# Optimization experiments

Measured on AMD Instinct MI355X. Metric: run time of the kernel, lower is better.

The kernel has to match this reference:

```python
import jax, jax.numpy as jnp
import numpy as np

EPS = 1e-6
N_HEADS = 16
KV_HEADS = 4
HEAD_DIM = 64
N_REP = N_HEADS // KV_HEADS
N_EXPERTS = 8
TOP_K = 2


def _rms_norm(x, w):
    return x * jax.lax.rsqrt(jnp.mean(x * x, axis=-1, keepdims=True) + EPS) * w


def _apply_rope(x, fc):
    # x: (B,T,H,D); fc: (T, D//2, 2) holding (cos, sin)
    B, T, H, D = x.shape
    xr = x.reshape(B, T, H, D // 2, 2)
    f = fc.reshape(1, T, 1, D // 2, 2)
    re = xr[..., 0] * f[..., 0] - xr[..., 1] * f[..., 1]
    im = xr[..., 1] * f[..., 0] + xr[..., 0] * f[..., 1]
    return jnp.stack([re, im], axis=-1).reshape(B, T, H, D)


def _silu(x):
    return x * jax.nn.sigmoid(x)


def setup_inputs():
    key = jax.random.key(0)
    ks = jax.random.split(key, 16)
    B, T, C = 4, 1024, 1024
    IE, IS = 1024, 2048  # expert_inter_dim, shared inter_dim
    s = 0.02
    x = jax.random.normal(ks[0], (B, T, C), jnp.float32)
    inv_freq = 1.0 / (10000.0 ** (np.arange(0, HEAD_DIM, 2, dtype=np.float32) / HEAD_DIM))
    ang = np.outer(np.arange(T, dtype=np.float32), inv_freq)
    freq_cis = jnp.asarray(np.stack([np.cos(ang), np.sin(ang)], axis=-1), jnp.float32)
    causal = np.tril(np.ones((T, T), dtype=bool))
    mask = jnp.asarray(np.where(causal, 0.0, -1e9), dtype=jnp.float32).reshape(1, 1, T, T)
    window = jnp.zeros((1, 1, T, T), jnp.float32)
    return {
        "x": x,
        "freq_cis": freq_cis,
        "mask": mask,
        "window": window,
        "norm1_w": jnp.ones((C,), jnp.float32),
        "wq": jax.random.normal(ks[1], (N_HEADS * HEAD_DIM, C), jnp.float32) * s,
        "wk": jax.random.normal(ks[2], (KV_HEADS * HEAD_DIM, C), jnp.float32) * s,
        "wv": jax.random.normal(ks[3], (KV_HEADS * HEAD_DIM, C), jnp.float32) * s,
        "wo": jax.random.normal(ks[4], (C, N_HEADS * HEAD_DIM), jnp.float32) * s,
        "norm2_w": jnp.ones((C,), jnp.float32),
        "gate_w": jax.random.normal(ks[5], (N_EXPERTS, C), jnp.float32) * s,
        "exp_w1": jax.random.normal(ks[6], (N_EXPERTS, IE, C), jnp.float32) * s,
        "exp_w2": jax.random.normal(ks[7], (N_EXPERTS, IE, C), jnp.float32) * s,
        "exp_wp": jax.random.normal(ks[8], (N_EXPERTS, C, IE), jnp.float32) * s,
        "sh_w1": jax.random.normal(ks[9], (IS, C), jnp.float32) * s,
        "sh_w2": jax.random.normal(ks[10], (IS, C), jnp.float32) * s,
        "sh_wp": jax.random.normal(ks[11], (C, IS), jnp.float32) * s,
        "start_pos": 0,
    }


def reference(x, freq_cis, mask, window, norm1_w, wq, wk, wv, wo, norm2_w,
              gate_w, exp_w1, exp_w2, exp_wp, sh_w1, sh_w2, sh_wp, start_pos):
    B, T, C = x.shape
    # ---- pre-norm attention (GQA, Global mask, eval: no dropout) ----
    xn = _rms_norm(x, norm1_w)
    q = (xn @ wq.T).reshape(B, T, N_HEADS, HEAD_DIM)
    k = (xn @ wk.T).reshape(B, T, KV_HEADS, HEAD_DIM)
    v = (xn @ wv.T).reshape(B, T, KV_HEADS, HEAD_DIM)
    q = _apply_rope(q, freq_cis)
    k = _apply_rope(k, freq_cis)
    k = jnp.repeat(k, N_REP, axis=2)  # (B,T,H,D)
    v = jnp.repeat(v, N_REP, axis=2)
    scale = 1.0 / np.sqrt(HEAD_DIM).astype(np.float32)
    att = jnp.einsum("bqhd,bkhd->bhqk", q, k) * scale + mask
    p = jax.nn.softmax(att, axis=-1)
    o = jnp.einsum("bhqk,bkhd->bqhd", p, v).reshape(B, T, C)
    x = x + o @ wo.T
    # ---- pre-norm MoE FFN ----
    xn2 = _rms_norm(x, norm2_w).reshape(-1, C)  # (N,C)
    scores = xn2 @ gate_w.T                      # gate logits, returned
    probs = jax.nn.softmax(scores, axis=-1)
    top_w, top_i = jax.lax.top_k(probs, TOP_K)   # (N,K)
    # dense combine weights (N,E): zero for non-selected experts
    wfull = jnp.sum(jax.nn.one_hot(top_i, N_EXPERTS, dtype=x.dtype) * top_w[..., None], axis=1)
    h = _silu(jnp.einsum("nc,eic->eni", xn2, exp_w1)) * jnp.einsum("nc,eic->eni", xn2, exp_w2)
    ye = jnp.einsum("eni,eci->enc", h, exp_wp)   # per-expert outputs
    y = jnp.einsum("ne,enc->nc", wfull, ye)      # routed combine
    z = (_silu(xn2 @ sh_w1.T) * (xn2 @ sh_w2.T)) @ sh_wp.T  # shared expert
    out = x + (y + z).reshape(B, T, C)
    return out, scores
```

## Files before the change

### kernel.cpp

```cpp
#include <hip/hip_runtime.h>


typedef __bf16 bf16_t;
typedef __bf16 bf16x8 __attribute__((ext_vector_type(8)));
typedef __bf16 bf16x4 __attribute__((ext_vector_type(4)));
typedef float  f32x4  __attribute__((ext_vector_type(4)));

#define LQKV 1536

#define GLD16(gp, lp) __builtin_amdgcn_global_load_lds(                         \
    (const __attribute__((address_space(1))) void*)(gp),                        \
    (__attribute__((address_space(3))) void*)(lp), 16, 0, 0)

#define PIPE_BARRIER() do {                                                     \
    asm volatile("s_waitcnt vmcnt(0)" ::: "memory");                            \
    __builtin_amdgcn_s_barrier();                                               \
} while (0)

__global__ __launch_bounds__(256) void convert_k(
    const float* __restrict__ src, bf16_t* __restrict__ dst)
{
    size_t i = (size_t)blockIdx.x * 256 + threadIdx.x;
    float4 v = *((const float4*)src + i);
    bf16x4 o;
    o[0] = (bf16_t)v.x; o[1] = (bf16_t)v.y; o[2] = (bf16_t)v.z; o[3] = (bf16_t)v.w;
    *((bf16x4*)dst + i) = o;
}

struct Cvt8 {
    const float* s[8];
    bf16_t* d[8];
    int cum[9];
    int nseg;
};

__global__ __launch_bounds__(256) void convert_multi_k(Cvt8 j)
{
    int blk = blockIdx.x;
    int seg = 0;
    while (seg + 1 < j.nseg && blk >= j.cum[seg + 1]) ++seg;
    size_t i = (size_t)(blk - j.cum[seg]) * 256 + threadIdx.x;
    float4 v = *((const float4*)j.s[seg] + i);
    bf16x4 o;
    o[0] = (bf16_t)v.x; o[1] = (bf16_t)v.y; o[2] = (bf16_t)v.z; o[3] = (bf16_t)v.w;
    *((bf16x4*)j.d[seg] + i) = o;
}

__global__ __launch_bounds__(256) void gemm_bt(
    const bf16_t* __restrict__ A, const bf16_t* __restrict__ W,
    int M, int N, int K, int ldw, int mode,
    float* __restrict__ outF, bf16_t* __restrict__ outB,
    const float* __restrict__ resF, float* __restrict__ outF2)
{
    __shared__ __align__(16) bf16_t sA[2][128 * 64];
    __shared__ __align__(16) bf16_t sB[2][128 * 64];
    const int tid  = threadIdx.x;
    const int bm   = blockIdx.y * 128, bn = blockIdx.x * 128;
    const int lane = tid & 63;
    const int wv   = tid >> 6;
    const int wm   = (wv >> 1) * 64, wn = (wv & 1) * 64;
    const int lr   = lane & 15;
    const int kg   = lane >> 4;
    const int swz  = (lr & 7) << 3;

    f32x4 acc[4][4];
    #pragma unroll
    for (int i = 0; i < 4; ++i)
        #pragma unroll
        for (int j = 0; j < 4; ++j)
            acc[i][j] = f32x4{0.f, 0.f, 0.f, 0.f};

    auto STAGE = [&](int b, int k0) {
        #pragma unroll
        for (int p = 0; p < 4; ++p) {
            int idx = p * 256 + tid;
            int row = idx >> 3;
            int ch  = ((idx & 7) * 8) ^ ((row & 7) << 3);
            GLD16(A + (size_t)(bm + row) * K   + k0 + ch, sA[b] + idx * 8);
            GLD16(W + (size_t)(bn + row) * ldw + k0 + ch, sB[b] + idx * 8);
        }
    };

    STAGE(0, 0);
    PIPE_BARRIER();
    int cur = 0;
    for (int k0 = 0; k0 < K; k0 += 64) {
        if (k0 + 64 < K) STAGE(cur ^ 1, k0 + 64);
        #pragma unroll
        for (int ks = 0; ks < 2; ++ks) {
            bf16x8 af[4], bfr[4];
            #pragma unroll
            for (int i = 0; i < 4; ++i)
                af[i] = *(const bf16x8*)(sA[cur] + (wm + i * 16 + lr) * 64 +
                                         ((ks * 32 + kg * 8) ^ swz));
            #pragma unroll
            for (int j = 0; j < 4; ++j)
                bfr[j] = *(const bf16x8*)(sB[cur] + (wn + j * 16 + lr) * 64 +
                                          ((ks * 32 + kg * 8) ^ swz));
            #pragma unroll
            for (int i = 0; i < 4; ++i)
                #pragma unroll
                for (int j = 0; j < 4; ++j)
                    acc[i][j] = __builtin_amdgcn_mfma_f32_16x16x32_bf16(
                        af[i], bfr[j], acc[i][j], 0, 0, 0);
        }
        PIPE_BARRIER();
        cur ^= 1;
    }

    #pragma unroll
    for (int i = 0; i < 4; ++i) {
        #pragma unroll
        for (int j = 0; j < 4; ++j) {
            #pragma unroll
            for (int rr = 0; rr < 4; ++rr) {
                int m = bm + wm + i * 16 + kg * 4 + rr;
                int n = bn + wn + j * 16 + lr;
                size_t o = (size_t)m * N + n;
                float v = acc[i][j][rr];
                if (mode == 0)      outF[o] = v;
                else if (mode == 1) outB[o] = (bf16_t)v;
                else if (mode == 2) {
                    float r = v + resF[o];
                    outF[o] = r;
                    if (outF2) outF2[o] = r;
                } else              outF[o] += v;
            }
        }
    }
}

__global__ __launch_bounds__(256) void gemm_glu(
    const bf16_t* __restrict__ A, const bf16_t* __restrict__ W1,
    const bf16_t* __restrict__ W2, int M, int N, int K,
    bf16_t* __restrict__ out)
{
    __shared__ __align__(16) bf16_t sA[2][128 * 64];
    __shared__ __align__(16) bf16_t sB1[2][128 * 64];
    __shared__ __align__(16) bf16_t sB2[2][128 * 64];
    const int tid  = threadIdx.x;
    const int bm   = blockIdx.y * 128, bn = blockIdx.x * 128;
    const int lane = tid & 63;
    const int wv   = tid >> 6;
    const int wm   = (wv >> 1) * 64, wn = (wv & 1) * 64;
    const int lr   = lane & 15;
    const int kg   = lane >> 4;
    const int swz  = (lr & 7) << 3;

    f32x4 acc1[4][4], acc2[4][4];
    #pragma unroll
    for (int i = 0; i < 4; ++i)
        #pragma unroll
        for (int j = 0; j < 4; ++j) {
            acc1[i][j] = f32x4{0.f, 0.f, 0.f, 0.f};
            acc2[i][j] = f32x4{0.f, 0.f, 0.f, 0.f};
        }

    auto STAGE = [&](int b, int k0) {
        #pragma unroll
        for (int p = 0; p < 4; ++p) {
            int idx = p * 256 + tid;
            int row = idx >> 3;
            int ch  = ((idx & 7) * 8) ^ ((row & 7) << 3);
            GLD16(A  + (size_t)(bm + row) * K + k0 + ch, sA[b]  + idx * 8);
            GLD16(W1 + (size_t)(bn + row) * K + k0 + ch, sB1[b] + idx * 8);
            GLD16(W2 + (size_t)(bn + row) * K + k0 + ch, sB2[b] + idx * 8);
        }
    };

    STAGE(0, 0);
    PIPE_BARRIER();
    int cur = 0;
    for (int k0 = 0; k0 < K; k0 += 64) {
        if (k0 + 64 < K) STAGE(cur ^ 1, k0 + 64);
        #pragma unroll
        for (int ks = 0; ks < 2; ++ks) {
            bf16x8 af[4], b1[4], b2[4];
            #pragma unroll
            for (int i = 0; i < 4; ++i)
                af[i] = *(const bf16x8*)(sA[cur] + (wm + i * 16 + lr) * 64 +
                                         ((ks * 32 + kg * 8) ^ swz));
            #pragma unroll
            for (int j = 0; j < 4; ++j) {
                b1[j] = *(const bf16x8*)(sB1[cur] + (wn + j * 16 + lr) * 64 +
                                         ((ks * 32 + kg * 8) ^ swz));
                b2[j] = *(const bf16x8*)(sB2[cur] + (wn + j * 16 + lr) * 64 +
                                         ((ks * 32 + kg * 8) ^ swz));
            }
            #pragma unroll
            for (int i = 0; i < 4; ++i)
                #pragma unroll
                for (int j = 0; j < 4; ++j) {
                    acc1[i][j] = __builtin_amdgcn_mfma_f32_16x16x32_bf16(
                        af[i], b1[j], acc1[i][j], 0, 0, 0);
                    acc2[i][j] = __builtin_amdgcn_mfma_f32_16x16x32_bf16(
                        af[i], b2[j], acc2[i][j], 0, 0, 0);
                }
        }
        PIPE_BARRIER();
        cur ^= 1;
    }

    #pragma unroll
    for (int i = 0; i < 4; ++i) {
        #pragma unroll
        for (int j = 0; j < 4; ++j) {
            #pragma unroll
            for (int rr = 0; rr < 4; ++rr) {
                int m = bm + wm + i * 16 + kg * 4 + rr;
                int n = bn + wn + j * 16 + lr;
                float v1 = acc1[i][j][rr], v2 = acc2[i][j][rr];
                out[(size_t)m * N + n] = (bf16_t)(v1 / (1.f + __expf(-v1)) * v2);
            }
        }
    }
}

__device__ __forceinline__ int seg_off(const int* cnt, int e)
{
    int r = 0;
    #pragma unroll
    for (int k = 0; k < 8; ++k) if (k < e) r += (cnt[k] + 127) & ~127;
    return r;
}

__global__ __launch_bounds__(256) void glu_gather(
    const bf16_t* __restrict__ A, const bf16_t* __restrict__ W1,
    const bf16_t* __restrict__ W2, const int* __restrict__ tok_list,
    const int* __restrict__ cnt, bf16_t* __restrict__ h)
{
    const int e = blockIdx.y >> 5, t = blockIdx.y & 31;
    const int ce = cnt[e];
    if (t * 128 >= ce) return;
    const int hbase = seg_off(cnt, e) + t * 128;
    const bf16_t* W1e = W1 + (size_t)e * 1048576;
    const bf16_t* W2e = W2 + (size_t)e * 1048576;

    __shared__ __align__(16) bf16_t sA[2][128 * 64];
    __shared__ __align__(16) bf16_t sB1[2][128 * 64];
    __shared__ __align__(16) bf16_t sB2[2][128 * 64];
    const int tid  = threadIdx.x;
    const int bn   = blockIdx.x * 128;
    const int lane = tid & 63;
    const int wv   = tid >> 6;
    const int wm   = (wv >> 1) * 64, wn = (wv & 1) * 64;
    const int lr   = lane & 15;
    const int kg   = lane >> 4;
    const int swz  = (lr & 7) << 3;

    int tok4[4];
    #pragma unroll
    for (int p = 0; p < 4; ++p)
        tok4[p] = tok_list[e * 4096 + t * 128 + ((p * 256 + tid) >> 3)];

    f32x4 acc1[4][4], acc2[4][4];
    #pragma unroll
    for (int i = 0; i < 4; ++i)
        #pragma unroll
        for (int j = 0; j < 4; ++j) {
            acc1[i][j] = f32x4{0.f, 0.f, 0.f, 0.f};
            acc2[i][j] = f32x4{0.f, 0.f, 0.f, 0.f};
        }

    auto STAGE = [&](int b, int k0) {
        #pragma unroll
        for (int p = 0; p < 4; ++p) {
            int idx = p * 256 + tid;
            int row = idx >> 3;
            int ch  = ((idx & 7) * 8) ^ ((row & 7) << 3);
            GLD16(A   + (size_t)tok4[p] * 1024 + k0 + ch,    sA[b]  + idx * 8);
            GLD16(W1e + (size_t)(bn + row) * 1024 + k0 + ch, sB1[b] + idx * 8);
            GLD16(W2e + (size_t)(bn + row) * 1024 + k0 + ch, sB2[b] + idx * 8);
        }
    };

    STAGE(0, 0);
    PIPE_BARRIER();
    int cur = 0;
    for (int k0 = 0; k0 < 1024; k0 += 64) {
        if (k0 + 64 < 1024) STAGE(cur ^ 1, k0 + 64);
        #pragma unroll
        for (int ks = 0; ks < 2; ++ks) {
            bf16x8 af[4], b1[4], b2[4];
            #pragma unroll
            for (int i = 0; i < 4; ++i)
                af[i] = *(const bf16x8*)(sA[cur] + (wm + i * 16 + lr) * 64 +
                                         ((ks * 32 + kg * 8) ^ swz));
            #pragma unroll
            for (int j = 0; j < 4; ++j) {
                b1[j] = *(const bf16x8*)(sB1[cur] + (wn + j * 16 + lr) * 64 +
                                         ((ks * 32 + kg * 8) ^ swz));
                b2[j] = *(const bf16x8*)(sB2[cur] + (wn + j * 16 + lr) * 64 +
                                         ((ks * 32 + kg * 8) ^ swz));
            }
            #pragma unroll
            for (int i = 0; i < 4; ++i)
                #pragma unroll
                for (int j = 0; j < 4; ++j) {
                    acc1[i][j] = __builtin_amdgcn_mfma_f32_16x16x32_bf16(
                        af[i], b1[j], acc1[i][j], 0, 0, 0);
                    acc2[i][j] = __builtin_amdgcn_mfma_f32_16x16x32_bf16(
                        af[i], b2[j], acc2[i][j], 0, 0, 0);
                }
        }
        PIPE_BARRIER();
        cur ^= 1;
    }

    #pragma unroll
    for (int i = 0; i < 4; ++i) {
        #pragma unroll
        for (int j = 0; j < 4; ++j) {
            #pragma unroll
            for (int rr = 0; rr < 4; ++rr) {
                int rl = wm + i * 16 + kg * 4 + rr;
                int n  = bn + wn + j * 16 + lr;
                float v1 = acc1[i][j][rr], v2 = acc2[i][j][rr];
                h[(size_t)(hbase + rl) * 1024 + n] =
                    (bf16_t)(v1 / (1.f + __expf(-v1)) * v2);
            }
        }
    }
}

__global__ __launch_bounds__(256) void down_gather(
    const bf16_t* __restrict__ h, const bf16_t* __restrict__ Wp,
    const int* __restrict__ tok_list, const float* __restrict__ w_list,
    const int* __restrict__ cnt, float* __restrict__ out)
{
    const int e = blockIdx.y >> 5, t = blockIdx.y & 31;
    const int ce = cnt[e];
    if (t * 128 >= ce) return;
    const int hbase = seg_off(cnt, e) + t * 128;
    const bf16_t* We = Wp + (size_t)e * 1048576;

    __shared__ __align__(16) bf16_t sA[2][128 * 64];
    __shared__ __align__(16) bf16_t sB[2][128 * 64];
    const int tid  = threadIdx.x;
    const int bn   = blockIdx.x * 128;
    const int lane = tid & 63;
    const int wv   = tid >> 6;
    const int wm   = (wv >> 1) * 64, wn = (wv & 1) * 64;
    const int lr   = lane & 15;
    const int kg   = lane >> 4;
    const int swz  = (lr & 7) << 3;

    f32x4 acc[4][4];
    #pragma unroll
    for (int i = 0; i < 4; ++i)
        #pragma unroll
        for (int j = 0; j < 4; ++j)
            acc[i][j] = f32x4{0.f, 0.f, 0.f, 0.f};

    auto STAGE = [&](int b, int k0) {
        #pragma unroll
        for (int p = 0; p < 4; ++p) {
            int idx = p * 256 + tid;
            int row = idx >> 3;
            int ch  = ((idx & 7) * 8) ^ ((row & 7) << 3);
            GLD16(h  + (size_t)(hbase + row) * 1024 + k0 + ch, sA[b] + idx * 8);
            GLD16(We + (size_t)(bn + row) * 1024 + k0 + ch,    sB[b] + idx * 8);
        }
    };

    STAGE(0, 0);
    PIPE_BARRIER();
    int cur = 0;
    for (int k0 = 0; k0 < 1024; k0 += 64) {
        if (k0 + 64 < 1024) STAGE(cur ^ 1, k0 + 64);
        #pragma unroll
        for (int ks = 0; ks < 2; ++ks) {
            bf16x8 af[4], bfr[4];
            #pragma unroll
            for (int i = 0; i < 4; ++i)
                af[i] = *(const bf16x8*)(sA[cur] + (wm + i * 16 + lr) * 64 +
                                         ((ks * 32 + kg * 8) ^ swz));
            #pragma unroll
            for (int j = 0; j < 4; ++j)
                bfr[j] = *(const bf16x8*)(sB[cur] + (wn + j * 16 + lr) * 64 +
                                          ((ks * 32 + kg * 8) ^ swz));
            #pragma unroll
            for (int i = 0; i < 4; ++i)
                #pragma unroll
                for (int j = 0; j < 4; ++j)
                    acc[i][j] = __builtin_amdgcn_mfma_f32_16x16x32_bf16(
                        af[i], bfr[j], acc[i][j], 0, 0, 0);
        }
        PIPE_BARRIER();
        cur ^= 1;
    }

    #pragma unroll
    for (int i = 0; i < 4; ++i) {
        #pragma unroll
        for (int rr = 0; rr < 4; ++rr) {
            int g = t * 128 + wm + i * 16 + kg * 4 + rr;
            if (g < ce) {
                int   tok = tok_list[e * 4096 + g];
                float wgt = w_list[e * 4096 + g];
                #pragma unroll
                for (int j = 0; j < 4; ++j) {
                    int n = bn + wn + j * 16 + lr;
                    atomicAdd(&out[(size_t)tok * 1024 + n], wgt * acc[i][j][rr]);
                }
            }
        }
    }
}

__global__ __launch_bounds__(256) void rmsnorm_k(
    const float* __restrict__ src, const float* __restrict__ w,
    bf16_t* __restrict__ dst)
{
    const int row = blockIdx.x, tid = threadIdx.x;
    float4 t4 = *((const float4*)src + (size_t)row * 256 + tid);
    float ssum = t4.x*t4.x + t4.y*t4.y + t4.z*t4.z + t4.w*t4.w;
    #pragma unroll
    for (int off = 32; off > 0; off >>= 1) ssum += __shfl_down(ssum, off);
    __shared__ float red[4];
    if ((tid & 63) == 0) red[tid >> 6] = ssum;
    __syncthreads();
    float total = red[0] + red[1] + red[2] + red[3];
    float rms = rsqrtf(total * (1.0f / 1024.0f) + 1e-6f);
    float4 w4 = *((const float4*)w + tid);
    bf16x4 o4;
    o4[0] = (bf16_t)(t4.x * rms * w4.x);
    o4[1] = (bf16_t)(t4.y * rms * w4.y);
    o4[2] = (bf16_t)(t4.z * rms * w4.z);
    o4[3] = (bf16_t)(t4.w * rms * w4.w);
    *((bf16x4*)dst + (size_t)row * 256 + tid) = o4;
}

__global__ __launch_bounds__(256) void rmsnorm_gate_k(
    const float* __restrict__ src, const float* __restrict__ w,
    const float* __restrict__ gw, bf16_t* __restrict__ dst,
    float* __restrict__ scores, int* __restrict__ topi,
    float* __restrict__ topw)
{
    const int row = blockIdx.x, tid = threadIdx.x;
    float4 t4 = *((const float4*)src + (size_t)row * 256 + tid);
    float ssum = t4.x*t4.x + t4.y*t4.y + t4.z*t4.z + t4.w*t4.w;
    #pragma unroll
    for (int off = 32; off > 0; off >>= 1) ssum += __shfl_down(ssum, off);
    __shared__ float red[4];
    if ((tid & 63) == 0) red[tid >> 6] = ssum;
    __syncthreads();
    float total = red[0] + red[1] + red[2] + red[3];
    float rms = rsqrtf(total * (1.0f / 1024.0f) + 1e-6f);
    float4 w4 = *((const float4*)w + tid);
    float4 f4;
    f4.x = t4.x * rms * w4.x;
    f4.y = t4.y * rms * w4.y;
    f4.z = t4.z * rms * w4.z;
    f4.w = t4.w * rms * w4.w;
    bf16x4 o4;
    o4[0] = (bf16_t)f4.x; o4[1] = (bf16_t)f4.y;
    o4[2] = (bf16_t)f4.z; o4[3] = (bf16_t)f4.w;
    *((bf16x4*)dst + (size_t)row * 256 + tid) = o4;

    float a[8];
    #pragma unroll
    for (int e = 0; e < 8; ++e) {
        float4 g4 = *((const float4*)(gw + (size_t)e * 1024) + tid);
        a[e] = f4.x * g4.x + f4.y * g4.y + f4.z * g4.z + f4.w * g4.w;
    }
    #pragma unroll
    for (int e = 0; e < 8; ++e)
        #pragma unroll
        for (int off = 32; off > 0; off >>= 1) a[e] += __shfl_down(a[e], off);
    __shared__ float gred[4][8];
    if ((tid & 63) == 0)
        #pragma unroll
        for (int e = 0; e < 8; ++e) gred[tid >> 6][e] = a[e];
    __syncthreads();
    if (tid == 0) {
        float lg[8];
        #pragma unroll
        for (int e = 0; e < 8; ++e)
            lg[e] = gred[0][e] + gred[1][e] + gred[2][e] + gred[3][e];
        #pragma unroll
        for (int e = 0; e < 8; ++e) scores[(size_t)row * 8 + e] = lg[e];
        float mx = lg[0];
        #pragma unroll
        for (int e = 1; e < 8; ++e) mx = fmaxf(mx, lg[e]);
        float p[8], sum = 0.f;
        #pragma unroll
        for (int e = 0; e < 8; ++e) { p[e] = __expf(lg[e] - mx); sum += p[e]; }
        float inv = 1.0f / sum;
        #pragma unroll
        for (int e = 0; e < 8; ++e) p[e] *= inv;
        int i1 = 0;
        #pragma unroll
        for (int e = 1; e < 8; ++e) if (p[e] > p[i1]) i1 = e;
        int i2 = (i1 == 0) ? 1 : 0;
        #pragma unroll
        for (int e = 0; e < 8; ++e) if (e != i1 && p[e] > p[i2]) i2 = e;
        topi[row] = i1 | (i2 << 8);
        topw[row * 2]     = p[i1];
        topw[row * 2 + 1] = p[i2];
    }
}

__global__ __launch_bounds__(256) void build_lists_k(
    const int* __restrict__ topi, const float* __restrict__ topw,
    int* __restrict__ tok_list, float* __restrict__ w_list,
    int* __restrict__ cnt)
{
    const int e = blockIdx.x;
    const int tid = threadIdx.x, lane = tid & 63, wv = tid >> 6;
    __shared__ int wc[4];
    int base = 0;
    for (int t0 = 0; t0 < 4096; t0 += 256) {
        int tok = t0 + tid;
        int ti = topi[tok];
        int i1 = ti & 255, i2 = (ti >> 8) & 255;
        bool m = (i1 == e) || (i2 == e);
        unsigned long long b = __ballot(m);
        if (lane == 0) wc[wv] = __popcll(b);
        __syncthreads();
        int pos = base;
        #pragma unroll
        for (int k = 0; k < 4; ++k) if (k < wv) pos += wc[k];
        pos += __popcll(b & ((1ull << lane) - 1ull));
        if (m) {
            tok_list[e * 4096 + pos] = tok;
            w_list[e * 4096 + pos]   = (i1 == e) ? topw[tok * 2] : topw[tok * 2 + 1];
        }
        base += wc[0] + wc[1] + wc[2] + wc[3];
        __syncthreads();
    }
    int padded = (base + 127) & ~127;
    for (int p = base + tid; p < padded; p += 256) tok_list[e * 4096 + p] = 0;
    if (tid == 0) cnt[e] = base;
}

__global__ __launch_bounds__(256) void rope_all_k(
    bf16_t* __restrict__ qkv, const float* __restrict__ fc)
{
    int idx = blockIdx.x * 256 + threadIdx.x;
    int pr = idx & 31;
    int hn = idx >> 5;
    int h  = hn % 20;
    int n  = hn / 20;
    int tpos = n & 1023;
    const float* f = fc + ((size_t)tpos * 32 + pr) * 2;
    float c = f[0], s = f[1];
    int col = (h < 16) ? h * 64 : 1024 + (h - 16) * 64;
    size_t base = (size_t)n * LQKV + col + pr * 2;
    float x0 = (float)qkv[base], x1 = (float)qkv[base + 1];
    qkv[base]     = (bf16_t)(x0 * c - x1 * s);
    qkv[base + 1] = (bf16_t)(x1 * c + x0 * s);
}

__global__ __launch_bounds__(256) void transpose_v(
    const bf16_t* __restrict__ qkv, bf16_t* __restrict__ vt)
{
    __shared__ bf16_t tile[64][72];
    const int tt = blockIdx.x, kvh = blockIdx.y, b = blockIdx.z;
    const int tid = threadIdx.x;
    {
        int r = tid >> 2, c = (tid & 3) * 16;
        const bf16_t* src = qkv + ((size_t)(b * 1024 + tt * 64 + r)) * LQKV
                            + 1280 + kvh * 64 + c;
        bf16x8 v0 = *(const bf16x8*)src;
        bf16x8 v1 = *(const bf16x8*)(src + 8);
        *(bf16x8*)&tile[r][c] = v0;
        *(bf16x8*)&tile[r][c + 8] = v1;
    }
    __syncthreads();
    {
        int d = tid >> 2, t4 = (tid & 3) * 16;
        bf16_t* dst = vt + ((size_t)((b * 4 + kvh) * 64 + d)) * 1024 + tt * 64 + t4;
        bf16x8 o0, o1;
        #pragma unroll
        for (int u = 0; u < 8; ++u) {
            o0[u] = tile[t4 + u][d];
            o1[u] = tile[t4 + 8 + u][d];
        }
        *(bf16x8*)dst = o0;
        *(bf16x8*)(dst + 8) = o1;
    }
}

__global__ __launch_bounds__(256) void attn_mfma(
    const bf16_t* __restrict__ qkv, const bf16_t* __restrict__ vt,
    bf16_t* __restrict__ ob)
{
    const int qt = blockIdx.x, h = blockIdx.y, b = blockIdx.z;
    const int kvh = h >> 2;
    __shared__ __align__(16) bf16_t sK[64 * 64];
    __shared__ __align__(16) bf16_t sVt[64 * 64];
    __shared__ __align__(16) bf16_t sP[64 * 72];
    const int tid  = threadIdx.x;
    const int w    = tid >> 6;
    const int lane = tid & 63;
    const int lr   = lane & 15;
    const int kg   = lane >> 4;
    const int swz  = (lr & 7) << 3;

    bf16x8 qf[2];
    {
        const bf16_t* qrow = qkv + ((size_t)(b * 1024 + qt * 64 + w * 16 + lr)) * LQKV
                             + h * 64;
        qf[0] = *(const bf16x8*)(qrow + kg * 8);
        qf[1] = *(const bf16x8*)(qrow + 32 + kg * 8);
    }
    float m_run[4], l_run[4];
    f32x4 o_acc[4];
    #pragma unroll
    for (int rr = 0; rr < 4; ++rr) { m_run[rr] = -1.0e30f; l_run[rr] = 0.f; }
    #pragma unroll
    for (int dt = 0; dt < 4; ++dt) o_acc[dt] = f32x4{0.f, 0.f, 0.f, 0.f};

    for (int kt = 0; kt <= qt; ++kt) {
        #pragma unroll
        for (int p = 0; p < 2; ++p) {
            int idx = p * 256 + tid;
            int row = idx >> 3;
            int chs = ((idx & 7) * 8) ^ ((row & 7) << 3);
            GLD16(qkv + ((size_t)(b * 1024 + kt * 64 + row)) * LQKV
                      + 1024 + kvh * 64 + chs, sK + idx * 8);
            GLD16(vt + ((size_t)((b * 4 + kvh) * 64 + row)) * 1024 + kt * 64 + chs,
                  sVt + idx * 8);
        }
        __syncthreads();

        f32x4 sfr[4];
        #pragma unroll
        for (int j = 0; j < 4; ++j) {
            sfr[j] = f32x4{0.f, 0.f, 0.f, 0.f};
            #pragma unroll
            for (int ks = 0; ks < 2; ++ks) {
                bf16x8 bf = *(const bf16x8*)(sK + (j * 16 + lr) * 64 +
                                             ((ks * 32 + kg * 8) ^ swz));
                sfr[j] = __builtin_amdgcn_mfma_f32_16x16x32_bf16(qf[ks], bf, sfr[j], 0, 0, 0);
            }
        }
        const int rowg = qt * 64 + w * 16 + kg * 4;
        float mnew[4];
        #pragma unroll
        for (int rr = 0; rr < 4; ++rr) mnew[rr] = m_run[rr];
        #pragma unroll
        for (int j = 0; j < 4; ++j) {
            int colg = kt * 64 + j * 16 + lr;
            #pragma unroll
            for (int rr = 0; rr < 4; ++rr) {
                float s = sfr[j][rr] * 0.125f;
                if (colg > rowg + rr) s = -1.0e30f;
                sfr[j][rr] = s;
                mnew[rr] = fmaxf(mnew[rr], s);
            }
        }
        #pragma unroll
        for (int off = 1; off < 16; off <<= 1)
            #pragma unroll
            for (int rr = 0; rr < 4; ++rr)
                mnew[rr] = fmaxf(mnew[rr], __shfl_xor(mnew[rr], off, 64));
        float alpha[4], lpart[4];
        #pragma unroll
        for (int rr = 0; rr < 4; ++rr) {
            alpha[rr] = __expf(m_run[rr] - mnew[rr]);
            lpart[rr] = 0.f;
        }
        #pragma unroll
        for (int j = 0; j < 4; ++j)
            #pragma unroll
            for (int rr = 0; rr < 4; ++rr) {
                float p = __expf(sfr[j][rr] - mnew[rr]);
                sfr[j][rr] = p;
                lpart[rr] += p;
            }
        #pragma unroll
        for (int j = 0; j < 4; ++j)
            #pragma unroll
            for (int rr = 0; rr < 4; ++rr)
                sP[(w * 16 + kg * 4 + rr) * 72 + j * 16 + lr] = (bf16_t)sfr[j][rr];
        #pragma unroll
        for (int off = 1; off < 16; off <<= 1)
            #pragma unroll
            for (int rr = 0; rr < 4; ++rr)
                lpart[rr] += __shfl_xor(lpart[rr], off, 64);
        #pragma unroll
        for (int rr = 0; rr < 4; ++rr) {
            l_run[rr] = l_run[rr] * alpha[rr] + lpart[rr];
            m_run[rr] = mnew[rr];
        }
        #pragma unroll
        for (int dt = 0; dt < 4; ++dt)
            #pragma unroll
            for (int rr = 0; rr < 4; ++rr)
                o_acc[dt][rr] *= alpha[rr];
        #pragma unroll
        for (int ks = 0; ks < 2; ++ks) {
            bf16x8 af = *(const bf16x8*)(sP + (w * 16 + lr) * 72 + ks * 32 + kg * 8);
            #pragma unroll
            for (int dt = 0; dt < 4; ++dt) {
                bf16x8 bf = *(const bf16x8*)(sVt + (dt * 16 + lr) * 64 +
                                             ((ks * 32 + kg * 8) ^ swz));
                o_acc[dt] = __builtin_amdgcn_mfma_f32_16x16x32_bf16(af, bf, o_acc[dt], 0, 0, 0);
            }
        }
        __syncthreads();
    }

    float inv[4];
    #pragma unroll
    for (int rr = 0; rr < 4; ++rr) inv[rr] = 1.0f / l_run[rr];
    #pragma unroll
    for (int dt = 0; dt < 4; ++dt)
        #pragma unroll
        for (int rr = 0; rr < 4; ++rr) {
            int tok = qt * 64 + w * 16 + kg * 4 + rr;
            ob[((size_t)(b * 1024 + tok)) * 1024 + h * 64 + dt * 16 + lr] =
                (bf16_t)(o_acc[dt][rr] * inv[rr]);
        }
}

extern "C" void kernel_launch(void* const* d_in, const int* in_sizes, int n_in,
                              void* d_out, int out_size, void* d_ws, size_t ws_size,
                              hipStream_t stream)
{
    const float* x   = (const float*)d_in[0];
    const float* fc  = (const float*)d_in[1];
    const float* n1w = (const float*)d_in[4];
    const float* wq  = (const float*)d_in[5];
    const float* wk  = (const float*)d_in[6];
    const float* wv  = (const float*)d_in[7];
    const float* wo  = (const float*)d_in[8];
    const float* n2w = (const float*)d_in[9];
    const float* gw  = (const float*)d_in[10];
    const float* ew1 = (const float*)d_in[11];
    const float* ew2 = (const float*)d_in[12];
    const float* ewp = (const float*)d_in[13];
    const float* sw1 = (const float*)d_in[14];
    const float* sw2 = (const float*)d_in[15];
    const float* swp = (const float*)d_in[16];

    const size_t MB = 1024 * 1024;
    char* ws = (char*)d_ws;
    bf16_t* xnb  = (bf16_t*)(ws + 0);
    float*  x1   = (float*) (ws + 8 * MB);
    bf16_t* ew2b = (bf16_t*)(ws + 8 * MB);
    bf16_t* h    = (bf16_t*)(ws + 24 * MB);
    char*   lists= ws + 42 * MB;
    int*    tok_list = (int*)lists;
    float*  w_list   = (float*)(lists + 131072);
    int*    cnt      = (int*)(lists + 262144);
    int*    topi     = (int*)(lists + 262400);
    float*  topw     = (float*)(lists + 278784);
    bf16_t* sw1b = (bf16_t*)(ws + 43 * MB);
    bf16_t* sw2b = (bf16_t*)(ws + 47 * MB);
    bf16_t* swpb = (bf16_t*)(ws + 51 * MB);
    char*   slotA= ws + 55 * MB;
    bf16_t* hb   = (bf16_t*)slotA;
    bf16_t* qkv  = (bf16_t*)(ws + 71 * MB);
    bf16_t* ob   = (bf16_t*)(ws + 83 * MB);
    bf16_t* vt   = (bf16_t*)(ws + 91 * MB);
    bf16_t* ew1b = (bf16_t*)(ws + 71 * MB);
    bf16_t* ewpb = (bf16_t*)(ws + 71 * MB);

    float* outp   = (float*)d_out;
    float* scores = outp + (size_t)4096 * 1024;

    auto gemm = [&](const bf16_t* A, const bf16_t* W, int M, int N, int K, int ldw,
                    int mode, float* oF, bf16_t* oB, const float* res, float* oF2) {
        gemm_bt<<<dim3(N / 128, M / 128), 256, 0, stream>>>(
            A, W, M, N, K, ldw, mode, oF, oB, res, oF2);
    };

    bf16_t* wqb = (bf16_t*)slotA;
    bf16_t* wkb = wqb + 1048576;
    bf16_t* wvb = wkb + 262144;
    bf16_t* wob = wvb + 262144;
    {
        Cvt8 j;
        j.s[0]=wq;  j.d[0]=wqb;  j.s[1]=wk;  j.d[1]=wkb;
        j.s[2]=wv;  j.d[2]=wvb;  j.s[3]=wo;  j.d[3]=wob;
        j.s[4]=sw1; j.d[4]=sw1b; j.s[5]=sw2; j.d[5]=sw2b;
        j.s[6]=swp; j.d[6]=swpb; j.s[7]=nullptr; j.d[7]=nullptr;
        int sz[7] = {1024, 256, 256, 1024, 2048, 2048, 2048};
        j.cum[0] = 0;
        for (int k = 0; k < 7; ++k) j.cum[k + 1] = j.cum[k] + sz[k];
        j.cum[8] = j.cum[7];
        j.nseg = 7;
        convert_multi_k<<<j.cum[7], 256, 0, stream>>>(j);
    }

    rmsnorm_k<<<4096, 256, 0, stream>>>(x, n1w, xnb);
    gemm(xnb, wqb, 4096, LQKV, 1024, 1024, 1, nullptr, qkv, nullptr, nullptr);
    rope_all_k<<<(4096 * 20 * 32) / 256, 256, 0, stream>>>(qkv, fc);
    transpose_v<<<dim3(16, 4, 4), 256, 0, stream>>>(qkv, vt);
    attn_mfma<<<dim3(16, 16, 4), 256, 0, stream>>>(qkv, vt, ob);
    gemm(ob, wob, 4096, 1024, 1024, 1024, 2, x1, nullptr, x, outp);

    rmsnorm_gate_k<<<4096, 256, 0, stream>>>(x1, n2w, gw, xnb, scores, topi, topw);
    build_lists_k<<<8, 256, 0, stream>>>(topi, topw, tok_list, w_list, cnt);

    {
        Cvt8 j;
        j.s[0]=ew1; j.d[0]=ew1b; j.s[1]=ew2; j.d[1]=ew2b;
        for (int k = 2; k < 8; ++k) { j.s[k]=nullptr; j.d[k]=nullptr; }
        j.cum[0] = 0; j.cum[1] = 8192; j.cum[2] = 16384;
        for (int k = 3; k < 9; ++k) j.cum[k] = 16384;
        j.nseg = 2;
        convert_multi_k<<<16384, 256, 0, stream>>>(j);
    }

    gemm_glu<<<dim3(16, 32), 256, 0, stream>>>(xnb, sw1b, sw2b, 4096, 2048, 1024, hb);
    glu_gather<<<dim3(8, 256), 256, 0, stream>>>(xnb, ew1b, ew2b, tok_list, cnt, h);

    convert_k<<<8192, 256, 0, stream>>>(ewp, ewpb);

    gemm(hb, swpb, 4096, 1024, 2048, 2048, 3, outp, nullptr, nullptr, nullptr);
    down_gather<<<dim3(8, 256), 256, 0, stream>>>(h, ewpb, tok_list, w_list, cnt, outp);

    (void)in_sizes; (void)n_in; (void)out_size; (void)ws_size;
}
```

Before: 617.5 us.

## Triple-buffer glu_gather with BK=32 and remap blocks to interleave experts

The gated expert GEMM moves from a double-buffered K=64 tile to a triple-buffered K=32 tile. Two stages are prefetched ahead, and partial vmcnt waits let global loads overlap compute across two iterations; the LDS swizzle is redesigned for the 32-wide rows. Both glu_gather and down_gather also remap the flat block index so experts are interleaved across consecutive workgroups, which should spread empty tiles and weight traffic more evenly. The cost is twice as many barriers per K, and the hard-coded vmcnt counts must match the number of loads issued per stage.

Measured after the change: 617.3 us. Within noise of the previous version (-0.0%).

```diff
diff --git a/kernel.cpp b/kernel.cpp
--- a/kernel.cpp
+++ b/kernel.cpp
@@ -14,6 +14,18 @@
 
 #define PIPE_BARRIER() do {                                                     \
     asm volatile("s_waitcnt vmcnt(0)" ::: "memory");                            \
+    __builtin_amdgcn_s_barrier();                                               \
+} while (0)
+
+#define WAIT_BAR(ahead, L2s, L1s) do {                                          \
+    if ((ahead) == 2)      asm volatile("s_waitcnt vmcnt(" L2s ")" ::: "memory");\
+    else if ((ahead) == 1) asm volatile("s_waitcnt vmcnt(" L1s ")" ::: "memory");\
+    else                   asm volatile("s_waitcnt vmcnt(0)" ::: "memory");     \
+    __builtin_amdgcn_s_barrier();                                               \
+} while (0)
+
+#define BAR_LGKM() do {                                                         \
+    asm volatile("s_waitcnt lgkmcnt(0)" ::: "memory");                          \
     __builtin_amdgcn_s_barrier();                                               \
 } while (0)
 
@@ -229,29 +241,32 @@
     const bf16_t* __restrict__ W2, const int* __restrict__ tok_list,
     const int* __restrict__ cnt, bf16_t* __restrict__ h)
 {
-    const int e = blockIdx.y >> 5, t = blockIdx.y & 31;
+    const int wg = blockIdx.y * 8 + blockIdx.x;
+    const int e  = wg & 7;
+    const int r_ = wg >> 3;
+    const int t  = r_ & 31;
+    const int bn = (r_ >> 5) * 128;
     const int ce = cnt[e];
     if (t * 128 >= ce) return;
     const int hbase = seg_off(cnt, e) + t * 128;
     const bf16_t* W1e = W1 + (size_t)e * 1048576;
     const bf16_t* W2e = W2 + (size_t)e * 1048576;
 
-    __shared__ __align__(16) bf16_t sA[2][128 * 64];
-    __shared__ __align__(16) bf16_t sB1[2][128 * 64];
-    __shared__ __align__(16) bf16_t sB2[2][128 * 64];
+    __shared__ __align__(16) bf16_t sA[3][128 * 32];
+    __shared__ __align__(16) bf16_t sB1[3][128 * 32];
+    __shared__ __align__(16) bf16_t sB2[3][128 * 32];
     const int tid  = threadIdx.x;
-    const int bn   = blockIdx.x * 128;
     const int lane = tid & 63;
     const int wv   = tid >> 6;
     const int wm   = (wv >> 1) * 64, wn = (wv & 1) * 64;
     const int lr   = lane & 15;
     const int kg   = lane >> 4;
-    const int swz  = (lr & 7) << 3;
-
-    int tok4[4];
-    #pragma unroll
-    for (int p = 0; p < 4; ++p)
-        tok4[p] = tok_list[e * 4096 + t * 128 + ((p * 256 + tid) >> 3)];
+    const int rsw  = (lr >> 1) & 3;
+
+    int tok2[2];
+    #pragma unroll
+    for (int p = 0; p < 2; ++p)
+        tok2[p] = tok_list[e * 4096 + t * 128 + ((p * 256 + tid) >> 2)];
 
     f32x4 acc1[4][4], acc2[4][4];
     #pragma unroll
@@ -264,47 +279,46 @@
 
     auto STAGE = [&](int b, int k0) {
         #pragma unroll
-        for (int p = 0; p < 4; ++p) {
+        for (int p = 0; p < 2; ++p) {
             int idx = p * 256 + tid;
-            int row = idx >> 3;
-            int ch  = ((idx & 7) * 8) ^ ((row & 7) << 3);
-            GLD16(A   + (size_t)tok4[p] * 1024 + k0 + ch,    sA[b]  + idx * 8);
+            int row = idx >> 2;
+            int ch  = 8 * ((idx & 3) ^ ((idx >> 3) & 3));
+            GLD16(A   + (size_t)tok2[p] * 1024 + k0 + ch,    sA[b]  + idx * 8);
             GLD16(W1e + (size_t)(bn + row) * 1024 + k0 + ch, sB1[b] + idx * 8);
             GLD16(W2e + (size_t)(bn + row) * 1024 + k0 + ch, sB2[b] + idx * 8);
         }
     };
 
     STAGE(0, 0);
-    PIPE_BARRIER();
-    int cur = 0;
-    for (int k0 = 0; k0 < 1024; k0 += 64) {
-        if (k0 + 64 < 1024) STAGE(cur ^ 1, k0 + 64);
-        #pragma unroll
-        for (int ks = 0; ks < 2; ++ks) {
-            bf16x8 af[4], b1[4], b2[4];
-            #pragma unroll
-            for (int i = 0; i < 4; ++i)
-                af[i] = *(const bf16x8*)(sA[cur] + (wm + i * 16 + lr) * 64 +
-                                         ((ks * 32 + kg * 8) ^ swz));
+    STAGE(1, 32);
+    int b0 = 0, b1 = 1, b2 = 2;
+    for (int kt = 0; kt < 32; ++kt) {
+        if (kt + 2 < 32) STAGE(b2, (kt + 2) * 32);
+        int ahead = (kt + 2 < 32) ? 2 : ((kt + 1 < 32) ? 1 : 0);
+        WAIT_BAR(ahead, "12", "6");
+        const bf16_t* sAr  = sA[b0];
+        const bf16_t* sB1r = sB1[b0];
+        const bf16_t* sB2r = sB2[b0];
+        bf16x8 af[4], f1[4], f2[4];
+        #pragma unroll
+        for (int i = 0; i < 4; ++i)
+            af[i] = *(const bf16x8*)(sAr + (wm + i * 16 + lr) * 32 + 8 * (kg ^ rsw));
+        #pragma unroll
+        for (int j = 0; j < 4; ++j) {
+            f1[j] = *(const bf16x8*)(sB1r + (wn + j * 16 + lr) * 32 + 8 * (kg ^ rsw));
+            f2[j] = *(const bf16x8*)(sB2r + (wn + j * 16 + lr) * 32 + 8 * (kg ^ rsw));
+        }
+        #pragma unroll
+        for (int i = 0; i < 4; ++i)
             #pragma unroll
             for (int j = 0; j < 4; ++j) {
-                b1[j] = *(const bf16x8*)(sB1[cur] + (wn + j * 16 + lr) * 64 +
-                                         ((ks * 32 + kg * 8) ^ swz));
-                b2[j] = *(const bf16x8*)(sB2[cur] + (wn + j * 16 + lr) * 64 +
-                                         ((ks * 32 + kg * 8) ^ swz));
-            }
-            #pragma unroll
-            for (int i = 0; i < 4; ++i)
-                #pragma unroll
-                for (int j = 0; j < 4; ++j) {
-                    acc1[i][j] = __builtin_amdgcn_mfma_f32_16x16x32_bf16(
-                        af[i], b1[j], acc1[i][j], 0, 0, 0);
-                    acc2[i][j] = __builtin_amdgcn_mfma_f32_16x16x32_bf16(
-                        af[i], b2[j], acc2[i][j], 0, 0, 0);
-                }
-        }
-        PIPE_BARRIER();
-        cur ^= 1;
+                acc1[i][j] = __builtin_amdgcn_mfma_f32_16x16x32_bf16(
+                    af[i], f1[j], acc1[i][j], 0, 0, 0);
+                acc2[i][j] = __builtin_amdgcn_mfma_f32_16x16x32_bf16(
+                    af[i], f2[j], acc2[i][j], 0, 0, 0);
+            }
+        BAR_LGKM();
+        int tt = b0; b0 = b1; b1 = b2; b2 = tt;
     }
 
     #pragma unroll
@@ -328,7 +342,11 @@
     const int* __restrict__ tok_list, const float* __restrict__ w_list,
     const int* __restrict__ cnt, float* __restrict__ out)
 {
-    const int e = blockIdx.y >> 5, t = blockIdx.y & 31;
+    const int wg = blockIdx.y * 8 + blockIdx.x;
+    const int e  = wg & 7;
+    const int r_ = wg >> 3;
+    const int t  = r_ & 31;
+    const int bn = (r_ >> 5) * 128;
     const int ce = cnt[e];
     if (t * 128 >= ce) return;
     const int hbase = seg_off(cnt, e) + t * 128;
@@ -337,7 +355,6 @@
     __shared__ __align__(16) bf16_t sA[2][128 * 64];
     __shared__ __align__(16) bf16_t sB[2][128 * 64];
     const int tid  = threadIdx.x;
-    const int bn   = blockIdx.x * 128;
     const int lane = tid & 63;
     const int wv   = tid >> 6;
     const int wm   = (wv >> 1) * 64, wn = (wv & 1) * 64;
```
